# Kernel tuning notes

Measured on AMD Instinct MI355X. Metric: run time of the kernel, lower is better.

Reference implementation:

```python
import jax, jax.numpy as jnp
import numpy as np

B, T, D, H = 4, 1024, 1024, 16
DH = D // H
NEG_BIG = jnp.float32(-2.0**32 + 1)


def layer_norm(x, scale, bias, eps=1e-5):
    mean = jnp.mean(x, axis=-1, keepdims=True)
    var = jnp.mean(jnp.square(x - mean), axis=-1, keepdims=True)
    return (x - mean) * jax.lax.rsqrt(var + eps) * scale + bias


def setup_inputs() -> dict:
    key = jax.random.key(0)
    ks = jax.random.split(key, 10)
    s = 0.02
    x = jax.random.normal(ks[0], (B, T, D), jnp.float32)
    mask = jax.random.randint(ks[1], (B, T), 0, 2).astype(jnp.float32)
    return {
        "x": x,
        "mask": mask,
        "wq": jax.random.normal(ks[2], (D, D), jnp.float32) * s,
        "wk": jax.random.normal(ks[3], (D, D), jnp.float32) * s,
        "wv": jax.random.normal(ks[4], (D, D), jnp.float32) * s,
        "w1": jax.random.normal(ks[5], (D, D), jnp.float32) * s,
        "b1": jnp.zeros((D,), jnp.float32),
        "w2": jax.random.normal(ks[6], (D, D), jnp.float32) * s,
        "b2": jnp.zeros((D,), jnp.float32),
        "ln1_s": jnp.ones((D,), jnp.float32),
        "ln1_b": jnp.zeros((D,), jnp.float32),
        "ln2_s": jnp.ones((D,), jnp.float32),
        "ln2_b": jnp.zeros((D,), jnp.float32),
        "ln3_s": jnp.ones((D,), jnp.float32),
        "ln3_b": jnp.zeros((D,), jnp.float32),
    }


def _mask_enc(x, mask, wq, wk, wv, w1, b1, w2, b2,
              ln1_s, ln1_b, ln2_s, ln2_b, ln3_s, ln3_b):
    b, t, d = x.shape
    # --- multi-head attention (hand-rolled, matches torch split/cat trick) ---
    Q = (x @ wq).reshape(b, t, H, DH).transpose(0, 2, 1, 3)  # [B,H,T,dh]
    K = (x @ wk).reshape(b, t, H, DH).transpose(0, 2, 1, 3)
    V = (x @ wv).reshape(b, t, H, DH).transpose(0, 2, 1, 3)
    scores = jnp.einsum('bhqd,bhkd->bhqk', Q, K) / jnp.sqrt(jnp.float32(DH))
    # key padding mask from sign of |K| row sums
    key_m = jnp.sign(jnp.sum(jnp.abs(K), axis=-1))  # [B,H,T]
    scores = jnp.where(key_m[:, :, None, :] == 0, NEG_BIG, scores)
    # FORWARD direction: allowed where col_index > row_index (strict)
    idx = jnp.arange(t)
    allowed = (idx[None, :] > idx[:, None]).astype(scores.dtype)  # [T,T]
    scores = scores + (1.0 - allowed) * (-10000.0)
    attn = jax.nn.softmax(scores, axis=-1)
    # post-softmax query mask multiply
    query_m = jnp.sign(jnp.sum(jnp.abs(Q), axis=-1))[:, :, :, None]  # [B,H,T,1]
    attn = attn * query_m
    out = jnp.einsum('bhqk,bhkd->bhqd', attn, V)
    out = out.transpose(0, 2, 1, 3).reshape(b, t, d)  # combine heads
    out = out * mask[:, :, None]
    # --- residual + layernorm wrapper (attention) ---
    h1 = layer_norm(x + out, ln1_s, ln1_b)
    # --- FFN + residual + layernorm ---
    ffn = jax.nn.relu(h1 @ w1 + b1) @ w2 + b2
    h2 = layer_norm(h1 + ffn, ln2_s, ln2_b)
    # --- output normalization ---
    return layer_norm(h2, ln3_s, ln3_b)


def reference(x, mask, wq, wk, wv, w1, b1, w2, b2,
              ln1_s, ln1_b, ln2_s, ln2_b, ln3_s, ln3_b):
    return _mask_enc(x, mask, wq, wk, wv, w1, b1, w2, b2,
                     ln1_s, ln1_b, ln2_s, ln2_b, ln3_s, ln3_b)
```

## Files before the change

### kernel.cpp

```cpp
#include <hip/hip_runtime.h>
#include <stdint.h>


#define B_  4
#define T_  1024
#define D_  1024
#define H_  16
#define DH_ 64

typedef __attribute__((ext_vector_type(8))) short short8;
typedef __attribute__((ext_vector_type(4))) float floatx4;
typedef __attribute__((ext_vector_type(4))) _Float16 half4;

__device__ __forceinline__ unsigned short f2bf(float f) {
  union { float f; uint32_t u; } a; a.f = f;
  uint32_t r = a.u + 0x7FFFu + ((a.u >> 16) & 1u);
  return (unsigned short)(r >> 16);
}
__device__ __forceinline__ float bf2f(unsigned short u) {
  union { uint32_t u; float f; } a; a.u = ((uint32_t)u) << 16;
  return a.f;
}

#define GLD_LDS16(g, l) __builtin_amdgcn_global_load_lds( \
    (const __attribute__((address_space(1))) unsigned int*)(g), \
    (__attribute__((address_space(3))) unsigned int*)(l), 16, 0, 0)

__global__ __launch_bounds__(256)
void prep_kernel(const float4* __restrict__ x4, unsigned short* __restrict__ xb,
                 const float* __restrict__ w0, const float* __restrict__ w1,
                 const float* __restrict__ w2, const float* __restrict__ w3,
                 const float* __restrict__ w4, unsigned short* __restrict__ dst_all) {
  const int t = threadIdx.x;
  if (blockIdx.x < 4096) {
    int idx = blockIdx.x * 256 + t;
    float4 v = x4[idx];
    union { uint2 u; unsigned short s[4]; } o;
    o.s[0] = f2bf(v.x); o.s[1] = f2bf(v.y); o.s[2] = f2bf(v.z); o.s[3] = f2bf(v.w);
    *(uint2*)&xb[(size_t)idx * 4] = o.u;
    return;
  }
  const int b = blockIdx.x - 4096;
  const int z = b >> 8, ky = (b >> 4) & 15, nx = b & 15;
  const float* src = (z == 0) ? w0 : (z == 1) ? w1 : (z == 2) ? w2 : (z == 3) ? w3 : w4;
  unsigned short* dst = dst_all + (size_t)z * D_ * D_;
  __shared__ __align__(16) unsigned short tile[64 * 72];
  const int k0 = ky * 64, n0 = nx * 64;
#pragma unroll
  for (int c = 0; c < 4; ++c) {
    int idx = c * 256 + t;
    int r = idx >> 4, cc = (idx & 15) << 2;
    float4 v = *(const float4*)&src[(size_t)(k0 + r) * D_ + n0 + cc];
    tile[(cc + 0) * 72 + r] = f2bf(v.x);
    tile[(cc + 1) * 72 + r] = f2bf(v.y);
    tile[(cc + 2) * 72 + r] = f2bf(v.z);
    tile[(cc + 3) * 72 + r] = f2bf(v.w);
  }
  __syncthreads();
  int rr = t >> 2, ck = (t & 3) << 4;
  uint4 v0 = *(const uint4*)&tile[rr * 72 + ck];
  uint4 v1 = *(const uint4*)&tile[rr * 72 + ck + 8];
  *(uint4*)&dst[(size_t)(n0 + rr) * D_ + k0 + ck] = v0;
  *(uint4*)&dst[(size_t)(n0 + rr) * D_ + k0 + ck + 8] = v1;
}

__global__ __launch_bounds__(256, 2)
void gemm_qkv(const unsigned short* __restrict__ A,
              const unsigned short* __restrict__ Bt,
              unsigned short* __restrict__ oQ, unsigned short* __restrict__ oK,
              _Float16* __restrict__ oV) {
  const int K = 1024;
  __shared__ __align__(16) unsigned short As[128 * 32];
  __shared__ __align__(16) unsigned short Bs[128 * 32];
  __shared__ __align__(16) _Float16 Cs[2 * 64 * 136];
  const int t = threadIdx.x;
  const int lane = t & 63, w = t >> 6;
  const int quad = lane >> 4, lm = lane & 15;
  const int wm = w >> 1, wn = w & 1;
  const int m0 = blockIdx.y * 128, n0 = blockIdx.x * 128;
  const int arow = w * 32 + (lane >> 2), acol = (lane & 3) << 3;

  floatx4 acc[4][4];
#pragma unroll
  for (int i = 0; i < 4; ++i)
#pragma unroll
    for (int j = 0; j < 4; ++j) acc[i][j] = (floatx4){0.f, 0.f, 0.f, 0.f};

  for (int kt = 0; kt < K; kt += 32) {
    const unsigned short* ga = A + (size_t)(m0 + arow) * K + kt + acol;
    const unsigned short* gb = Bt + (size_t)(n0 + arow) * K + kt + acol;
    GLD_LDS16(ga, &As[(w * 32) * 32]);
    GLD_LDS16(ga + (size_t)16 * K, &As[(w * 32 + 16) * 32]);
    GLD_LDS16(gb, &Bs[(w * 32) * 32]);
    GLD_LDS16(gb + (size_t)16 * K, &Bs[(w * 32 + 16) * 32]);
    __syncthreads();
    short8 a[4], b[4];
#pragma unroll
    for (int i = 0; i < 4; ++i) a[i] = *(const short8*)&As[(wm * 64 + i * 16 + lm) * 32 + quad * 8];
#pragma unroll
    for (int j = 0; j < 4; ++j) b[j] = *(const short8*)&Bs[(wn * 64 + j * 16 + lm) * 32 + quad * 8];
#pragma unroll
    for (int i = 0; i < 4; ++i)
#pragma unroll
      for (int j = 0; j < 4; ++j)
        acc[i][j] = __builtin_amdgcn_mfma_f32_16x16x32_bf16(a[i], b[j], acc[i][j], 0, 0, 0);
    __syncthreads();
  }

  if (n0 < 2048) {
    unsigned short* p = (n0 < 1024) ? oQ : oK;
    const float qscale = (n0 < 1024) ? 0.18033688f : 1.0f;
#pragma unroll
    for (int i = 0; i < 4; ++i) {
      int gmb = m0 + wm * 64 + i * 16 + quad * 4;
#pragma unroll
      for (int j = 0; j < 4; ++j) {
        int gn = n0 + wn * 64 + j * 16 + lm;
        int nn = gn & 1023, hh = nn >> 6, dd = nn & 63;
#pragma unroll
        for (int r = 0; r < 4; ++r) {
          int gm = gmb + r;
          int bb = gm >> 10, tt = gm & 1023;
          p[(((size_t)bb * H_ + hh) * T_ + tt) * DH_ + dd] = f2bf(acc[i][j][r] * qscale);
        }
      }
    }
  } else {
#pragma unroll
    for (int i = 0; i < 4; ++i) {
#pragma unroll
      for (int j = 0; j < 4; ++j) {
        int gn = n0 + wn * 64 + j * 16 + lm;
        int hd = (gn >> 6) & 1, dd = gn & 63;
        int kperm = quad * 32 + (wm * 4 + i) * 4;
        union { _Float16 h[4]; uint2 u; } pk;
#pragma unroll
        for (int r = 0; r < 4; ++r) pk.h[r] = (_Float16)acc[i][j][r];
        *(uint2*)&Cs[((size_t)(hd * 64 + dd)) * 136 + kperm] = pk.u;
      }
    }
    __syncthreads();
    const int row = t >> 1, half = t & 1;
    const int hd = row >> 6, dd = row & 63;
    const int hh = ((n0 & 1023) >> 6) + hd;
    const int bb = m0 >> 10, kbg = (m0 >> 7) & 7;
    const _Float16* srcp = &Cs[(size_t)(hd * 64 + dd) * 136 + half * 64];
    _Float16* dstp = oV + ((((size_t)bb * H_ + hh) * DH_ + dd) * 8 + kbg) * 128 + half * 64;
#pragma unroll
    for (int g = 0; g < 8; ++g)
      *(uint4*)(dstp + g * 8) = *(const uint4*)(srcp + g * 8);
  }
}

template <int MODE>
__global__ __launch_bounds__(256, 2)
void gemm_ffn(const unsigned short* __restrict__ A,
              const unsigned short* __restrict__ Bt,
              unsigned short* __restrict__ oBf, float* __restrict__ oF,
              const float* __restrict__ bias) {
  const int K = 1024, N = 1024;
  __shared__ __align__(16) unsigned short As[64 * 32];
  __shared__ __align__(16) unsigned short Bs[128 * 32];
  const int t = threadIdx.x;
  const int lane = t & 63, w = t >> 6;
  const int quad = lane >> 4, lm = lane & 15;
  const int wm = w >> 1, wn = w & 1;
  const int m0 = blockIdx.y * 64, n0 = blockIdx.x * 128;
  const int lrow = lane >> 2, lcol = (lane & 3) << 3;

  floatx4 acc[2][4];
#pragma unroll
  for (int i = 0; i < 2; ++i)
#pragma unroll
    for (int j = 0; j < 4; ++j) acc[i][j] = (floatx4){0.f, 0.f, 0.f, 0.f};

  for (int kt = 0; kt < K; kt += 32) {
    const unsigned short* ga = A + (size_t)(m0 + w * 16 + lrow) * K + kt + lcol;
    const unsigned short* gb = Bt + (size_t)(n0 + w * 32 + lrow) * K + kt + lcol;
    GLD_LDS16(ga, &As[(w * 16) * 32]);
    GLD_LDS16(gb, &Bs[(w * 32) * 32]);
    GLD_LDS16(gb + (size_t)16 * K, &Bs[(w * 32 + 16) * 32]);
    __syncthreads();
    short8 a[2], b[4];
#pragma unroll
    for (int i = 0; i < 2; ++i) a[i] = *(const short8*)&As[(wm * 32 + i * 16 + lm) * 32 + quad * 8];
#pragma unroll
    for (int j = 0; j < 4; ++j) b[j] = *(const short8*)&Bs[(wn * 64 + j * 16 + lm) * 32 + quad * 8];
#pragma unroll
    for (int i = 0; i < 2; ++i)
#pragma unroll
      for (int j = 0; j < 4; ++j)
        acc[i][j] = __builtin_amdgcn_mfma_f32_16x16x32_bf16(a[i], b[j], acc[i][j], 0, 0, 0);
    __syncthreads();
  }

#pragma unroll
  for (int i = 0; i < 2; ++i) {
    int gmb = m0 + wm * 32 + i * 16 + quad * 4;
#pragma unroll
    for (int j = 0; j < 4; ++j) {
      int gn = n0 + wn * 64 + j * 16 + lm;
      float bv = bias[gn];
#pragma unroll
      for (int r = 0; r < 4; ++r) {
        int gm = gmb + r;
        float v = acc[i][j][r] + bv;
        if (MODE == 1) {
          oBf[(size_t)gm * N + gn] = f2bf(fmaxf(v, 0.f));
        } else {
          oF[(size_t)gm * N + gn] = v;
        }
      }
    }
  }
}

__global__ __launch_bounds__(256)
void flash_attn(const unsigned short* __restrict__ Qb,
                const unsigned short* __restrict__ Kb,
                const _Float16* __restrict__ Vtg,
                const float* __restrict__ maskp,
                unsigned short* __restrict__ attn) {
  const int t = threadIdx.x;
  const int lane = t & 63, w = t >> 6;
  const int quad = lane >> 4, lm = lane & 15;

  const int bid = blockIdx.x;
  const int hi  = bid >> 8;
  const int lo  = bid & 255;
  const int xcd = lo & 7;
  const int hgrp = (lo >> 3) & 7;
  const int qpair = lo >> 6;
  const int qb = hi ? (7 - qpair) : qpair;
  const int head = hgrp * 8 + xcd;
  const int hh = head & 15, bb = head >> 4;
  const int q0 = qb << 7;

  const size_t headoff = ((size_t)bb * H_ + hh) * T_ * DH_;
  const unsigned short* Qh = Qb + headoff;
  const unsigned short* Kh = Kb + headoff;
  const _Float16* Vh = Vtg + headoff;

  short8 qf[2][2];
#pragma unroll
  for (int qg = 0; qg < 2; ++qg)
#pragma unroll
    for (int ks = 0; ks < 2; ++ks)
      qf[qg][ks] = *(const short8*)(Qh + (size_t)(q0 + w * 32 + qg * 16 + lm) * 64 + ks * 32 + quad * 8);

  float lsum[2] = {0.f, 0.f};
  floatx4 acc[2][4];
#pragma unroll
  for (int qg = 0; qg < 2; ++qg)
#pragma unroll
    for (int j2 = 0; j2 < 4; ++j2) acc[qg][j2] = (floatx4){0.f, 0.f, 0.f, 0.f};

  const int qglob0 = q0 + w * 32 + lm;
  const bool excl1 = (qglob0 + 16 == 1023);
  const float MSHIFT = 14426.950408f;

  const int kb_lo = (qb == 7 && w == 3) ? 0 : qb;

  short8 kf[8][2];
  {
    const unsigned short* Kblk = Kh + (size_t)(kb_lo * 128) * 64;
#pragma unroll
    for (int j = 0; j < 8; ++j) {
      kf[j][0] = *(const short8*)(Kblk + (size_t)(j * 16 + lm) * 64 + quad * 8);
      kf[j][1] = *(const short8*)(Kblk + (size_t)(j * 16 + lm) * 64 + 32 + quad * 8);
    }
  }

  for (int kb = kb_lo; kb < 8; ++kb) {
    const int k0 = kb * 128;
    const bool need_mask = (kb <= qb);
    const bool has_next = (kb + 1 < 8);
    const unsigned short* Kn = Kh + (size_t)((kb + 1) * 128) * 64;

    union { uint4 u[4]; _Float16 h[32]; } vf[4];
#pragma unroll
    for (int j2 = 0; j2 < 4; ++j2) {
      const _Float16* vp = Vh + ((size_t)(j2 * 16 + lm) * 8 + kb) * 128 + quad * 32;
#pragma unroll
      for (int g = 0; g < 4; ++g) vf[j2].u[g] = *(const uint4*)(vp + g * 8);
    }

#pragma unroll
    for (int j = 0; j < 8; ++j) {
      floatx4 st[2];
#pragma unroll
      for (int qg = 0; qg < 2; ++qg) {
        floatx4 z = (floatx4){0.f, 0.f, 0.f, 0.f};
        z = __builtin_amdgcn_mfma_f32_16x16x32_bf16(kf[j][0], qf[qg][0], z, 0, 0, 0);
        st[qg] = __builtin_amdgcn_mfma_f32_16x16x32_bf16(kf[j][1], qf[qg][1], z, 0, 0, 0);
      }
      if (has_next) {
        kf[j][0] = *(const short8*)(Kn + (size_t)(j * 16 + lm) * 64 + quad * 8);
        kf[j][1] = *(const short8*)(Kn + (size_t)(j * 16 + lm) * 64 + 32 + quad * 8);
      }
      half4 pa[2];
#pragma unroll
      for (int qg = 0; qg < 2; ++qg) {
        const int qq = qglob0 + qg * 16;
        const bool skip = (qg == 1) && excl1;
#pragma unroll
        for (int r = 0; r < 4; ++r) {
          int kg = k0 + j * 16 + quad * 4 + r;
          float v = st[qg][r];
          if (need_mask && !skip && kg <= qq) v -= MSHIFT;
          float p = __builtin_amdgcn_exp2f(v);
          lsum[qg] += p;
          pa[qg][r] = (_Float16)p;
        }
      }
#pragma unroll
      for (int j2 = 0; j2 < 4; ++j2) {
        half4 vb;
#pragma unroll
        for (int r = 0; r < 4; ++r) vb[r] = vf[j2].h[j * 4 + r];
        acc[0][j2] = __builtin_amdgcn_mfma_f32_16x16x16f16(pa[0], vb, acc[0][j2], 0, 0, 0);
        acc[1][j2] = __builtin_amdgcn_mfma_f32_16x16x16f16(pa[1], vb, acc[1][j2], 0, 0, 0);
      }
    }
  }

#pragma unroll
  for (int qg = 0; qg < 2; ++qg) {
    float l = lsum[qg];
    l += __shfl_xor(l, 16);
    l += __shfl_xor(l, 32);
    float s = maskp[bb * T_ + qglob0 + qg * 16] / l;
#pragma unroll
    for (int r = 0; r < 4; ++r) {
      float bsc = __shfl(s, quad * 4 + r);
      int tq = q0 + w * 32 + qg * 16 + quad * 4 + r;
#pragma unroll
      for (int j2 = 0; j2 < 4; ++j2)
        attn[((size_t)(bb * T_ + tq)) * D_ + hh * 64 + j2 * 16 + lm] = f2bf(acc[qg][j2][r] * bsc);
    }
  }
}

__global__ __launch_bounds__(256)
void ln_res_kernel(const float* __restrict__ xa, const unsigned short* __restrict__ attn,
                   const float* __restrict__ sc, const float* __restrict__ bi,
                   float* __restrict__ h, unsigned short* __restrict__ hb) {
  const int row = blockIdx.x, t = threadIdx.x;
  const int lane = t & 63, wid = t >> 6;
  size_t base = (size_t)row * D_ + t * 4;
  float4 a = *(const float4*)&xa[base];
  union { uint2 u; unsigned short s[4]; } au;
  au.u = *(const uint2*)&attn[base];
  float v0 = a.x + bf2f(au.s[0]), v1 = a.y + bf2f(au.s[1]);
  float v2 = a.z + bf2f(au.s[2]), v3 = a.w + bf2f(au.s[3]);
  float s1 = v0 + v1 + v2 + v3;
  float s2 = v0 * v0 + v1 * v1 + v2 * v2 + v3 * v3;
#pragma unroll
  for (int off = 32; off; off >>= 1) { s1 += __shfl_down(s1, off); s2 += __shfl_down(s2, off); }
  __shared__ float r1[4], r2[4];
  if (lane == 0) { r1[wid] = s1; r2[wid] = s2; }
  __syncthreads();
  s1 = r1[0] + r1[1] + r1[2] + r1[3];
  s2 = r2[0] + r2[1] + r2[2] + r2[3];
  float mean = s1 * (1.f / 1024.f);
  float var = s2 * (1.f / 1024.f) - mean * mean;
  float rstd = rsqrtf(var + 1e-5f);
  float4 sv = *(const float4*)&sc[t * 4];
  float4 bv = *(const float4*)&bi[t * 4];
  float o0 = (v0 - mean) * rstd * sv.x + bv.x;
  float o1 = (v1 - mean) * rstd * sv.y + bv.y;
  float o2 = (v2 - mean) * rstd * sv.z + bv.z;
  float o3 = (v3 - mean) * rstd * sv.w + bv.w;
  float4 ov = {o0, o1, o2, o3};
  *(float4*)&h[base] = ov;
  union { uint2 u; unsigned short s[4]; } ob;
  ob.s[0] = f2bf(o0); ob.s[1] = f2bf(o1); ob.s[2] = f2bf(o2); ob.s[3] = f2bf(o3);
  *(uint2*)&hb[base] = ob.u;
}

__global__ __launch_bounds__(256)
void ln_double_kernel(const float* __restrict__ h1, const float* __restrict__ ffn,
                      const float* __restrict__ s2c, const float* __restrict__ b2c,
                      const float* __restrict__ s3c, const float* __restrict__ b3c,
                      float* __restrict__ out) {
  const int row = blockIdx.x, t = threadIdx.x;
  const int lane = t & 63, wid = t >> 6;
  size_t base = (size_t)row * D_ + t * 4;
  float4 a = *(const float4*)&h1[base];
  float4 b = *(const float4*)&ffn[base];
  float v0 = a.x + b.x, v1 = a.y + b.y, v2 = a.z + b.z, v3 = a.w + b.w;
  float s1 = v0 + v1 + v2 + v3;
  float s2 = v0 * v0 + v1 * v1 + v2 * v2 + v3 * v3;
#pragma unroll
  for (int off = 32; off; off >>= 1) { s1 += __shfl_down(s1, off); s2 += __shfl_down(s2, off); }
  __shared__ float ra[4], rb[4], rc[4], rd[4];
  if (lane == 0) { ra[wid] = s1; rb[wid] = s2; }
  __syncthreads();
  s1 = ra[0] + ra[1] + ra[2] + ra[3];
  s2 = rb[0] + rb[1] + rb[2] + rb[3];
  float mean = s1 * (1.f / 1024.f);
  float var = s2 * (1.f / 1024.f) - mean * mean;
  float rstd = rsqrtf(var + 1e-5f);
  float4 sv = *(const float4*)&s2c[t * 4];
  float4 bv = *(const float4*)&b2c[t * 4];
  float o0 = (v0 - mean) * rstd * sv.x + bv.x;
  float o1 = (v1 - mean) * rstd * sv.y + bv.y;
  float o2 = (v2 - mean) * rstd * sv.z + bv.z;
  float o3 = (v3 - mean) * rstd * sv.w + bv.w;
  float u1 = o0 + o1 + o2 + o3;
  float u2 = o0 * o0 + o1 * o1 + o2 * o2 + o3 * o3;
#pragma unroll
  for (int off = 32; off; off >>= 1) { u1 += __shfl_down(u1, off); u2 += __shfl_down(u2, off); }
  if (lane == 0) { rc[wid] = u1; rd[wid] = u2; }
  __syncthreads();
  u1 = rc[0] + rc[1] + rc[2] + rc[3];
  u2 = rd[0] + rd[1] + rd[2] + rd[3];
  float mean2 = u1 * (1.f / 1024.f);
  float var2 = u2 * (1.f / 1024.f) - mean2 * mean2;
  float rstd2 = rsqrtf(var2 + 1e-5f);
  float4 s3v = *(const float4*)&s3c[t * 4];
  float4 b3v = *(const float4*)&b3c[t * 4];
  float4 fo;
  fo.x = (o0 - mean2) * rstd2 * s3v.x + b3v.x;
  fo.y = (o1 - mean2) * rstd2 * s3v.y + b3v.y;
  fo.z = (o2 - mean2) * rstd2 * s3v.z + b3v.z;
  fo.w = (o3 - mean2) * rstd2 * s3v.w + b3v.w;
  *(float4*)&out[base] = fo;
}

extern "C" void kernel_launch(void* const* d_in, const int* in_sizes, int n_in,
                              void* d_out, int out_size, void* d_ws, size_t ws_size,
                              hipStream_t stream) {
  (void)in_sizes; (void)n_in; (void)out_size; (void)ws_size;
  const float* x   = (const float*)d_in[0];
  const float* msk = (const float*)d_in[1];
  const float* wq  = (const float*)d_in[2];
  const float* wk  = (const float*)d_in[3];
  const float* wv  = (const float*)d_in[4];
  const float* w1  = (const float*)d_in[5];
  const float* b1  = (const float*)d_in[6];
  const float* w2  = (const float*)d_in[7];
  const float* b2  = (const float*)d_in[8];
  const float* l1s = (const float*)d_in[9];
  const float* l1b = (const float*)d_in[10];
  const float* l2s = (const float*)d_in[11];
  const float* l2b = (const float*)d_in[12];
  const float* l3s = (const float*)d_in[13];
  const float* l3b = (const float*)d_in[14];
  float* outp = (float*)d_out;

  char* ws = (char*)d_ws;
  unsigned short* xb   = (unsigned short*)(ws);
  unsigned short* wt   = (unsigned short*)(ws + ((size_t)8  << 20));
  unsigned short* Qb   = (unsigned short*)(ws + ((size_t)18 << 20));
  unsigned short* Kb   = (unsigned short*)(ws + ((size_t)26 << 20));
  _Float16*       Vtg  = (_Float16*)(ws + ((size_t)34 << 20));
  unsigned short* attn = (unsigned short*)(ws + ((size_t)42 << 20));
  float* h1            = (float*)(ws + ((size_t)50 << 20));
  unsigned short* h1b  = (unsigned short*)(ws + ((size_t)18 << 20));
  unsigned short* gb   = (unsigned short*)(ws + ((size_t)26 << 20));
  float* ffn           = (float*)(ws + ((size_t)34 << 20));

  prep_kernel<<<4096 + 1280, 256, 0, stream>>>((const float4*)x, xb,
                                               wq, wk, wv, w1, w2, wt);
  gemm_qkv<<<dim3(24, 32), 256, 0, stream>>>(xb, wt, Qb, Kb, Vtg);
  flash_attn<<<512, 256, 0, stream>>>(Qb, Kb, Vtg, msk, attn);
  ln_res_kernel<<<4096, 256, 0, stream>>>(x, attn, l1s, l1b, h1, h1b);
  gemm_ffn<1><<<dim3(8, 64), 256, 0, stream>>>(h1b, wt + (size_t)3 * 1024 * 1024, gb, nullptr, b1);
  gemm_ffn<2><<<dim3(8, 64), 256, 0, stream>>>(gb, wt + (size_t)4 * 1024 * 1024, nullptr, ffn, b2);
  ln_double_kernel<<<4096, 256, 0, stream>>>(h1, ffn, l2s, l2b, l3s, l3b, outp);
}
```

Baseline: 246.9 us.

## Stage K/V tiles through double-buffered LDS with async global-to-LDS loads

In flash attention, each wave used to load its own K and V tiles from global memory into registers. Now the four waves of a block share K/V tiles, staged in a double-buffered shared-memory ring with global_load_lds. The next tile is prefetched while the current one is computed, and fragments are read from LDS one step ahead. This cuts redundant global traffic across waves and overlaps loads with MFMA work, at the cost of a block-wide barrier per key block and 64KB of LDS, which may reduce occupancy.

```diff
diff --git a/kernel.cpp b/kernel.cpp
--- a/kernel.cpp
+++ b/kernel.cpp
@@ -221,6 +221,9 @@
                 const _Float16* __restrict__ Vtg,
                 const float* __restrict__ maskp,
                 unsigned short* __restrict__ attn) {
+  __shared__ __align__(16) unsigned short KLs[2][8192];
+  __shared__ __align__(16) _Float16      VLs[2][8192];
+
   const int t = threadIdx.x;
   const int lane = t & 63, w = t >> 6;
   const int quad = lane >> 4, lm = lane & 15;
@@ -259,69 +262,96 @@
   const bool excl1 = (qglob0 + 16 == 1023);
   const float MSHIFT = 14426.950408f;
 
-  const int kb_lo = (qb == 7 && w == 3) ? 0 : qb;
-
-  short8 kf[8][2];
-  {
-    const unsigned short* Kblk = Kh + (size_t)(kb_lo * 128) * 64;
-#pragma unroll
-    for (int j = 0; j < 8; ++j) {
-      kf[j][0] = *(const short8*)(Kblk + (size_t)(j * 16 + lm) * 64 + quad * 8);
-      kf[j][1] = *(const short8*)(Kblk + (size_t)(j * 16 + lm) * 64 + 32 + quad * 8);
-    }
-  }
-
-  for (int kb = kb_lo; kb < 8; ++kb) {
-    const int k0 = kb * 128;
-    const bool need_mask = (kb <= qb);
-    const bool has_next = (kb + 1 < 8);
-    const unsigned short* Kn = Kh + (size_t)((kb + 1) * 128) * 64;
-
-    union { uint4 u[4]; _Float16 h[32]; } vf[4];
-#pragma unroll
-    for (int j2 = 0; j2 < 4; ++j2) {
-      const _Float16* vp = Vh + ((size_t)(j2 * 16 + lm) * 8 + kb) * 128 + quad * 32;
-#pragma unroll
-      for (int g = 0; g < 4; ++g) vf[j2].u[g] = *(const uint4*)(vp + g * 8);
-    }
-
-#pragma unroll
-    for (int j = 0; j < 8; ++j) {
-      floatx4 st[2];
-#pragma unroll
-      for (int qg = 0; qg < 2; ++qg) {
-        floatx4 z = (floatx4){0.f, 0.f, 0.f, 0.f};
-        z = __builtin_amdgcn_mfma_f32_16x16x32_bf16(kf[j][0], qf[qg][0], z, 0, 0, 0);
-        st[qg] = __builtin_amdgcn_mfma_f32_16x16x32_bf16(kf[j][1], qf[qg][1], z, 0, 0, 0);
-      }
-      if (has_next) {
-        kf[j][0] = *(const short8*)(Kn + (size_t)(j * 16 + lm) * 64 + quad * 8);
-        kf[j][1] = *(const short8*)(Kn + (size_t)(j * 16 + lm) * 64 + 32 + quad * 8);
-      }
-      half4 pa[2];
-#pragma unroll
-      for (int qg = 0; qg < 2; ++qg) {
-        const int qq = qglob0 + qg * 16;
-        const bool skip = (qg == 1) && excl1;
-#pragma unroll
-        for (int r = 0; r < 4; ++r) {
-          int kg = k0 + j * 16 + quad * 4 + r;
-          float v = st[qg][r];
-          if (need_mask && !skip && kg <= qq) v -= MSHIFT;
-          float p = __builtin_amdgcn_exp2f(v);
-          lsum[qg] += p;
-          pa[qg][r] = (_Float16)p;
-        }
-      }
-#pragma unroll
-      for (int j2 = 0; j2 < 4; ++j2) {
-        half4 vb;
-#pragma unroll
-        for (int r = 0; r < 4; ++r) vb[r] = vf[j2].h[j * 4 + r];
-        acc[0][j2] = __builtin_amdgcn_mfma_f32_16x16x16f16(pa[0], vb, acc[0][j2], 0, 0, 0);
-        acc[1][j2] = __builtin_amdgcn_mfma_f32_16x16x16f16(pa[1], vb, acc[1][j2], 0, 0, 0);
+  const int my_lo  = (qb == 7 && w == 3) ? 0 : qb;
+  const int blk_lo = (qb == 7) ? 0 : qb;
+
+  const unsigned short* gk[4];
+  const _Float16* gv[4];
+#pragma unroll
+  for (int i = 0; i < 4; ++i) {
+    int s = w * 4 + i;
+    gk[i] = Kh + (size_t)((s >> 1) * 16 + lm) * 64 + (s & 1) * 32 + quad * 8;
+    gv[i] = Vh + ((size_t)((s >> 2) * 16 + lm) * 8) * 128 + quad * 32 + (s & 3) * 8;
+  }
+
+#pragma unroll
+  for (int i = 0; i < 4; ++i) {
+    int s = w * 4 + i;
+    GLD_LDS16(gk[i] + (size_t)blk_lo * 8192, &KLs[0][s * 512]);
+    GLD_LDS16(gv[i] + (size_t)blk_lo * 128,  &VLs[0][s * 512]);
+  }
+
+  int cur = 0;
+  for (int kb = blk_lo; kb < 8; ++kb) {
+    __syncthreads();
+    if (kb + 1 < 8) {
+      int nxt = cur ^ 1;
+#pragma unroll
+      for (int i = 0; i < 4; ++i) {
+        int s = w * 4 + i;
+        GLD_LDS16(gk[i] + (size_t)(kb + 1) * 8192, &KLs[nxt][s * 512]);
+        GLD_LDS16(gv[i] + (size_t)(kb + 1) * 128,  &VLs[nxt][s * 512]);
       }
     }
+    if (kb >= my_lo) {
+      const unsigned short* Kc = &KLs[cur][0];
+      const _Float16* Vc = &VLs[cur][0];
+      const int k0 = kb * 128;
+      const bool need_mask = (kb <= qb);
+
+      short8 kA = *(const short8*)&Kc[(0 * 64 + lane) * 8];
+      short8 kB = *(const short8*)&Kc[(1 * 64 + lane) * 8];
+      half4 vA0 = *(const half4*)&Vc[((0 * 4 + 0) * 64 + lane) * 8];
+      half4 vA1 = *(const half4*)&Vc[((1 * 4 + 0) * 64 + lane) * 8];
+      half4 vA2 = *(const half4*)&Vc[((2 * 4 + 0) * 64 + lane) * 8];
+      half4 vA3 = *(const half4*)&Vc[((3 * 4 + 0) * 64 + lane) * 8];
+
+#pragma unroll
+      for (int j = 0; j < 8; ++j) {
+        short8 nA, nB; half4 n0, n1, n2, n3;
+        if (j < 7) {
+          int jn = j + 1;
+          nA = *(const short8*)&Kc[((jn * 2 + 0) * 64 + lane) * 8];
+          nB = *(const short8*)&Kc[((jn * 2 + 1) * 64 + lane) * 8];
+          n0 = *(const half4*)&Vc[((0 * 4 + (jn >> 1)) * 64 + lane) * 8 + (jn & 1) * 4];
+          n1 = *(const half4*)&Vc[((1 * 4 + (jn >> 1)) * 64 + lane) * 8 + (jn & 1) * 4];
+          n2 = *(const half4*)&Vc[((2 * 4 + (jn >> 1)) * 64 + lane) * 8 + (jn & 1) * 4];
+          n3 = *(const half4*)&Vc[((3 * 4 + (jn >> 1)) * 64 + lane) * 8 + (jn & 1) * 4];
+        }
+        floatx4 st[2];
+#pragma unroll
+        for (int qg = 0; qg < 2; ++qg) {
+          floatx4 z = (floatx4){0.f, 0.f, 0.f, 0.f};
+          z = __builtin_amdgcn_mfma_f32_16x16x32_bf16(kA, qf[qg][0], z, 0, 0, 0);
+          st[qg] = __builtin_amdgcn_mfma_f32_16x16x32_bf16(kB, qf[qg][1], z, 0, 0, 0);
+        }
+        half4 pa[2];
+#pragma unroll
+        for (int qg = 0; qg < 2; ++qg) {
+          const int qq = qglob0 + qg * 16;
+          const bool skip = (qg == 1) && excl1;
+#pragma unroll
+          for (int r = 0; r < 4; ++r) {
+            int kg = k0 + j * 16 + quad * 4 + r;
+            float v = st[qg][r];
+            if (need_mask && !skip && kg <= qq) v -= MSHIFT;
+            float p = __builtin_amdgcn_exp2f(v);
+            lsum[qg] += p;
+            pa[qg][r] = (_Float16)p;
+          }
+        }
+        acc[0][0] = __builtin_amdgcn_mfma_f32_16x16x16f16(pa[0], vA0, acc[0][0], 0, 0, 0);
+        acc[1][0] = __builtin_amdgcn_mfma_f32_16x16x16f16(pa[1], vA0, acc[1][0], 0, 0, 0);
+        acc[0][1] = __builtin_amdgcn_mfma_f32_16x16x16f16(pa[0], vA1, acc[0][1], 0, 0, 0);
+        acc[1][1] = __builtin_amdgcn_mfma_f32_16x16x16f16(pa[1], vA1, acc[1][1], 0, 0, 0);
+        acc[0][2] = __builtin_amdgcn_mfma_f32_16x16x16f16(pa[0], vA2, acc[0][2], 0, 0, 0);
+        acc[1][2] = __builtin_amdgcn_mfma_f32_16x16x16f16(pa[1], vA2, acc[1][2], 0, 0, 0);
+        acc[0][3] = __builtin_amdgcn_mfma_f32_16x16x16f16(pa[0], vA3, acc[0][3], 0, 0, 0);
+        acc[1][3] = __builtin_amdgcn_mfma_f32_16x16x16f16(pa[1], vA3, acc[1][3], 0, 0, 0);
+        kA = nA; kB = nB; vA0 = n0; vA1 = n1; vA2 = n2; vA3 = n3;
+      }
+    }
+    cur ^= 1;
   }
 
 #pragma unroll
```

After: 235.1 us. 4.8% less time.
